# Kernel tuning notes

Hardware: AMD Instinct MI355X
Metric: run time of the kernel (lower is better)

The kernel has to match this reference:

```python
import jax, jax.numpy as jnp
import numpy as np

B, S, D, E = 8, 2048, 1024, 8
TOKENS = B * S
CAPACITY = TOKENS // E  # capacity_factor=1.0, top-1 gating (deepspeed default)


def _moe_layer(x_flat, Wg, We, be):
    """DeepSpeed-style top-1 MoE: gate -> capacity drop -> dispatch -> expert GEMM -> combine.
    x_flat: [T, D]; Wg: [D, E]; We: [E, D, D]; be: [E, D]."""
    gates = jax.nn.softmax(x_flat @ Wg, axis=-1)              # [T, E]
    idx = jnp.argmax(gates, axis=1)                            # [T] expert per token
    mask = jax.nn.one_hot(idx, E, dtype=jnp.int32)             # [T, E]
    loc = jnp.cumsum(mask, axis=0) - 1                         # position within expert
    loc_s = jnp.sum(loc * mask, axis=1)                        # [T]
    keep = loc_s < CAPACITY                                    # capacity drop
    gate_s = jnp.sum(gates * mask.astype(gates.dtype), axis=1) * keep.astype(gates.dtype)
    slot = jnp.clip(loc_s, 0, CAPACITY - 1)
    # dispatch: scatter kept tokens into [E, C, D] buffer (slots are unique for kept tokens)
    disp = jnp.zeros((E, CAPACITY, D), x_flat.dtype).at[idx, slot].add(
        x_flat * keep[:, None].astype(x_flat.dtype))
    # grouped expert GEMM
    eo = jnp.einsum('ecd,edf->ecf', disp, We) + be[:, None, :]  # [E, C, D]
    # combine: gather each token's expert output, scale by its gate value
    return eo[idx, slot] * gate_s[:, None]                      # [T, D]


def reference(x, y, W1, b1, Wg2, We2, be2, Wg3, We3, be3):
    h = jnp.einsum('bsd,df->bsf', x, W1) + b1                  # dense pre-layer
    hf = h.reshape(TOKENS, D)
    o = _moe_layer(hf, Wg2, We2, be2)
    o = _moe_layer(o, Wg3, We3, be3)
    h = h + o.reshape(B, S, D)                                 # residual add
    sent = h.mean(axis=1)                                      # [B, D]
    logp = jax.nn.log_softmax(sent, axis=-1)
    return -jnp.mean(logp[jnp.arange(B), y])                   # CrossEntropyLoss


def setup_inputs() -> dict:
    key = jax.random.key(0)
    ks = jax.random.split(key, 10)
    s = 0.02
    return {
        'x': jax.random.normal(ks[0], (B, S, D), jnp.float32),
        'y': jax.random.randint(ks[1], (B,), 0, D),
        'W1': jax.random.normal(ks[2], (D, D), jnp.float32) * s,
        'b1': jnp.zeros((D,), jnp.float32),
        'Wg2': jax.random.normal(ks[3], (D, E), jnp.float32) * s,
        'We2': jax.random.normal(ks[4], (E, D, D), jnp.float32) * s,
        'be2': jnp.zeros((E, D), jnp.float32),
        'Wg3': jax.random.normal(ks[5], (D, E), jnp.float32) * s,
        'We3': jax.random.normal(ks[6], (E, D, D), jnp.float32) * s,
        'be3': jnp.zeros((E, D), jnp.float32),
    }
```

## Files before the change

### kernel.cpp

```cpp
#include <hip/hip_runtime.h>
#include <hip/hip_bf16.h>
#include <math.h>


#define TOKS 16384
#define DIM 1024
#define NEXP 8
#define CAP 2048
#define BATCH 8
#define SEQ 2048

typedef __bf16 bf16_t;
typedef __bf16 bf16x8 __attribute__((ext_vector_type(8)));
typedef float fx4 __attribute__((ext_vector_type(4)));

__device__ __forceinline__ void gll16(const bf16_t* g, bf16_t* l) {
  __builtin_amdgcn_global_load_lds(
      (const __attribute__((address_space(1))) unsigned int*)g,
      (__attribute__((address_space(3))) unsigned int*)l, 16, 0, 0);
}

#define BARRIER() asm volatile("s_barrier" ::: "memory")
#define LGKM0()   asm volatile("s_waitcnt lgkmcnt(0)" ::: "memory")
#define VMC(N)    asm volatile("s_waitcnt vmcnt(" #N ")" ::: "memory")

#define PW_BLOCKS (17 * 64)
__global__ __launch_bounds__(256) void k_prep_w(
    const float* __restrict__ W1, const float* __restrict__ We2,
    const float* __restrict__ We3, bf16_t* __restrict__ Wt) {
  __shared__ bf16_t T[256][68];
  const int id = blockIdx.x;
  const int tid = threadIdx.x;
  const int m = id >> 6, rem = id & 63;
  const int k0 = (rem >> 4) * 256, n0 = (rem & 15) * 64;
  const float* src = (m == 0) ? W1
                     : (m <= 8) ? We2 + (size_t)(m - 1) * DIM * DIM
                                : We3 + (size_t)(m - 9) * DIM * DIM;
  bf16_t* dst = Wt + (size_t)m * DIM * DIM;
  const int r = tid >> 4, nq = tid & 15;
#pragma unroll
  for (int i = 0; i < 16; i++) {
    const int k = i * 16 + r;
    float4 v = *(const float4*)&src[(size_t)(k0 + k) * DIM + n0 + nq * 4];
    union { bf16_t h[4]; uint2 u; } t;
    t.h[0] = (bf16_t)v.x; t.h[1] = (bf16_t)v.y;
    t.h[2] = (bf16_t)v.z; t.h[3] = (bf16_t)v.w;
    *(uint2*)&T[k][(nq ^ ((k >> 3) & 15)) << 2] = t.u;
  }
  __syncthreads();
#pragma unroll
  for (int p = 0; p < 8; p++) {
    const int idx2 = p * 256 + tid;
    const int nl = idx2 >> 5, ks = (idx2 & 31) * 8;
    union { bf16_t h[8]; uint4 u; } o;
#pragma unroll
    for (int j = 0; j < 8; j++) {
      const int k = ks + j;
      o.h[j] = T[k][((((nl >> 2) ^ ((k >> 3) & 15)) << 2) | (nl & 3))];
    }
    *(uint4*)&dst[(size_t)(n0 + nl) * DIM + k0 + ks] = o.u;
  }
}

#define CVT_BLOCKS (TOKS * DIM / 8 / 256)
#define PREPX_GRID (2 + CVT_BLOCKS + 1)
__global__ __launch_bounds__(256) void k_prep_x(
    const float* __restrict__ Wg2, const float* __restrict__ Wg3,
    const float* __restrict__ x, bf16_t* __restrict__ WgP,
    bf16_t* __restrict__ xb, uint4* __restrict__ zreg, int znq) {
  const int id = blockIdx.x;
  const int tid = threadIdx.x;
  if (id < 2) {
    const int which = id;
    const float* src = which ? Wg3 : Wg2;
    bf16_t* dst = WgP + which * (128 * 8 * 8);
#pragma unroll
    for (int j = 0; j < 4; j++) {
      int d = tid * 4 + j;
      float4 a = *(const float4*)&src[d * 8];
      float4 b = *(const float4*)&src[d * 8 + 4];
      float v[8] = {a.x, a.y, a.z, a.w, b.x, b.y, b.z, b.w};
#pragma unroll
      for (int e = 0; e < 8; e++)
        dst[((d >> 3) * 8 + e) * 8 + (d & 7)] = (bf16_t)v[e];
    }
  } else if (id < 2 + CVT_BLOCKS) {
    const int cid = id - 2;
    size_t i = ((size_t)cid * 256 + tid) * 8;
    float4 a = *(const float4*)&x[i];
    float4 b = *(const float4*)&x[i + 4];
    union { bf16_t h[8]; uint4 u; } t;
    t.h[0] = (bf16_t)a.x; t.h[1] = (bf16_t)a.y; t.h[2] = (bf16_t)a.z; t.h[3] = (bf16_t)a.w;
    t.h[4] = (bf16_t)b.x; t.h[5] = (bf16_t)b.y; t.h[6] = (bf16_t)b.z; t.h[7] = (bf16_t)b.w;
    *(uint4*)&xb[i] = t.u;
  } else {
    const uint4 z = {0u, 0u, 0u, 0u};
    for (int i = tid; i < znq; i += 256) zreg[i] = z;
  }
}

template <int MODE>
__global__ __launch_bounds__(512) void k_gemm256(
    const bf16_t* __restrict__ A, const bf16_t* __restrict__ Bt0,
    const float* __restrict__ bias0, bf16_t* __restrict__ out,
    float* __restrict__ sent, const int* __restrict__ tok,
    const int* __restrict__ cnt, const float* __restrict__ gate,
    const bf16_t* __restrict__ zp) {
  __shared__ alignas(16) bf16_t As[2][256 * 64];
  __shared__ alignas(16) bf16_t Bs[2][256 * 64];
  const int tid = threadIdx.x;
  const int lane = tid & 63, wave = tid >> 6;
  const int quad = lane >> 4, l15 = lane & 15;
  const int wm = wave >> 2, wn = wave & 3;
  const int id = blockIdx.x;
  const int xcd = id & 7, rem = id >> 3;
  const int n0 = (rem & 3) * 256;

  int m0;
  int count = 0;
  const bf16_t* Bt;
  const float* bias;
  const int* tk = nullptr;
  if constexpr (MODE == 0) {
    m0 = (xcd * 8 + (rem >> 2)) * 256;
    Bt = Bt0;
    bias = bias0;
  } else {
    m0 = (rem >> 2) * 256;
    count = cnt[xcd];
    if (m0 >= count) return;
    Bt = Bt0 + (size_t)xcd * DIM * DIM;
    bias = bias0 + xcd * DIM;
    tk = tok + xcd * CAP;
  }

  const int kc = (tid & 7) ^ ((tid >> 3) & 7);
  const int rbase = tid >> 3;

  const bf16_t* gA[4];
  const bf16_t* gB[4];
#pragma unroll
  for (int h = 0; h < 2; h++)
#pragma unroll
    for (int i = 0; i < 2; i++) {
      const int r = h * 128 + i * 64 + rbase;
      if constexpr (MODE == 0) {
        gA[h * 2 + i] = A + (size_t)(m0 + r) * DIM + kc * 8;
      } else {
        const int ca = m0 + r;
        gA[h * 2 + i] = (ca < count) ? A + (size_t)tk[ca] * DIM + kc * 8 : zp;
      }
      gB[h * 2 + i] = Bt + (size_t)(n0 + r) * DIM + kc * 8;
    }

  auto stA = [&](int t, int half) {
#pragma unroll
    for (int i = 0; i < 2; i++)
      gll16(gA[half * 2 + i] + t * 64,
            &As[t & 1][(half * 128 + i * 64 + wave * 8) * 64]);
  };
  auto stB = [&](int t, int half) {
#pragma unroll
    for (int i = 0; i < 2; i++)
      gll16(gB[half * 2 + i] + t * 64,
            &Bs[t & 1][(half * 128 + i * 64 + wave * 8) * 64]);
  };
  auto rdA = [&](bf16x8 (&av)[4][2], int buf, int mh) {
#pragma unroll
    for (int mf = 0; mf < 4; mf++)
#pragma unroll
      for (int s = 0; s < 2; s++)
        av[mf][s] = *(const bf16x8*)&As[buf][(wm * 128 + (mh * 4 + mf) * 16 + l15) * 64 +
                                            (((s * 4 + quad) ^ (l15 & 7)) << 3)];
  };
  auto rdB = [&](bf16x8 (&bv)[2][2], int buf, int nh) {
#pragma unroll
    for (int nf = 0; nf < 2; nf++)
#pragma unroll
      for (int s = 0; s < 2; s++)
        bv[nf][s] = *(const bf16x8*)&Bs[buf][(wn * 64 + (nh * 2 + nf) * 16 + l15) * 64 +
                                            (((s * 4 + quad) ^ (l15 & 7)) << 3)];
  };

  fx4 acc[8][4];
#pragma unroll
  for (int i = 0; i < 8; i++)
#pragma unroll
    for (int j = 0; j < 4; j++) acc[i][j] = (fx4)0.0f;

  auto mma = [&](bf16x8 (&av)[4][2], bf16x8 (&bv)[2][2], int mh, int nh) {
    __builtin_amdgcn_s_setprio(1);
#pragma unroll
    for (int s = 0; s < 2; s++)
#pragma unroll
      for (int mf = 0; mf < 4; mf++)
#pragma unroll
        for (int nf = 0; nf < 2; nf++)
          acc[mh * 4 + mf][nh * 2 + nf] = __builtin_amdgcn_mfma_f32_16x16x32_bf16(
              av[mf][s], bv[nf][s], acc[mh * 4 + mf][nh * 2 + nf], 0, 0, 0);
    __builtin_amdgcn_s_setprio(0);
  };

  stA(0, 0); stA(0, 1); stB(0, 0); stB(0, 1);
  stB(1, 0); stB(1, 1); stA(1, 0);
  VMC(6);
  BARRIER();

  bf16x8 av0[4][2], av1[4][2], bv0[2][2], bv1[2][2];
#pragma unroll 2
  for (int t = 0; t < 14; t++) {
    const int buf = t & 1;
    rdA(av0, buf, 0); rdB(bv0, buf, 0); rdB(bv1, buf, 1);
    stA(t + 1, 1);
    BARRIER(); LGKM0();
    mma(av0, bv0, 0, 0);
    BARRIER();
    stB(t + 2, 0);
    BARRIER();
    mma(av0, bv1, 0, 1);
    BARRIER();
    rdA(av1, buf, 1);
    stB(t + 2, 1);
    BARRIER(); LGKM0();
    mma(av1, bv1, 1, 1);
    BARRIER();
    stA(t + 2, 0);
    mma(av1, bv0, 1, 0);
    VMC(6);
    BARRIER();
  }
  {
    rdA(av0, 0, 0); rdB(bv0, 0, 0); rdB(bv1, 0, 1);
    stA(15, 1);
    BARRIER(); LGKM0();
    mma(av0, bv0, 0, 0);
    BARRIER();
    mma(av0, bv1, 0, 1);
    BARRIER();
    rdA(av1, 0, 1);
    BARRIER(); LGKM0();
    mma(av1, bv1, 1, 1);
    BARRIER();
    mma(av1, bv0, 1, 0);
    VMC(0);
    BARRIER();
  }
  {
    rdA(av0, 1, 0); rdB(bv0, 1, 0); rdB(bv1, 1, 1); rdA(av1, 1, 1);
    LGKM0();
    mma(av0, bv0, 0, 0); mma(av0, bv1, 0, 1);
    mma(av1, bv1, 1, 1); mma(av1, bv0, 1, 0);
  }

  float bb[4];
#pragma unroll
  for (int nf = 0; nf < 4; nf++) bb[nf] = bias[n0 + wn * 64 + nf * 16 + l15];
  if constexpr (MODE == 0) {
    float sj[4] = {0.f, 0.f, 0.f, 0.f};
#pragma unroll
    for (int mf = 0; mf < 8; mf++)
#pragma unroll
      for (int r = 0; r < 4; r++) {
        const int rowL = wm * 128 + mf * 16 + quad * 4 + r;
#pragma unroll
        for (int nf = 0; nf < 4; nf++) {
          const float v = acc[mf][nf][r] + bb[nf];
          sj[nf] += v;
          out[(size_t)(m0 + rowL) * DIM + n0 + wn * 64 + nf * 16 + l15] = (bf16_t)v;
        }
      }
#pragma unroll
    for (int nf = 0; nf < 4; nf++) {
      sj[nf] += __shfl_xor(sj[nf], 16);
      sj[nf] += __shfl_xor(sj[nf], 32);
    }
    if (quad == 0)
#pragma unroll
      for (int nf = 0; nf < 4; nf++)
        atomicAdd(&sent[(m0 >> 11) * DIM + n0 + wn * 64 + nf * 16 + l15],
                  sj[nf] * (1.0f / SEQ));
  } else {
#pragma unroll
    for (int mf = 0; mf < 8; mf++)
#pragma unroll
      for (int r = 0; r < 4; r++) {
        const int c = m0 + wm * 128 + mf * 16 + quad * 4 + r;
        if (c < count) {
          const int tkn = tk[c];
          const float g = gate[tkn];
#pragma unroll
          for (int nf = 0; nf < 4; nf++)
            out[(size_t)tkn * DIM + n0 + wn * 64 + nf * 16 + l15] =
                (bf16_t)((acc[mf][nf][r] + bb[nf]) * g);
        }
      }
  }
}

__global__ __launch_bounds__(256) void k_gate_mm(
    const bf16_t* __restrict__ act, const bf16_t* __restrict__ WgPx,
    int* __restrict__ idx, float* __restrict__ gate) {
  __shared__ alignas(16) bf16_t As[64 * 64];
  __shared__ alignas(16) bf16_t WgS[128 * 64];
  __shared__ float L[64][8];
  const int tid = threadIdx.x;
  const int lane = tid & 63, wave = tid >> 6;
  const int quad = lane >> 4, l15 = lane & 15;
  const int m0 = blockIdx.x * 64;
  const int kc = (tid & 7) ^ ((tid >> 3) & 7);
  const int rbase = tid >> 3;

#pragma unroll
  for (int j = 0; j < 4; j++)
    gll16(WgPx + (j * 256 + wave * 64 + lane) * 8, &WgS[(j * 256 + wave * 64) * 8]);

  const bf16_t* gA[2]; bf16_t* lA[2];
#pragma unroll
  for (int i = 0; i < 2; i++) {
    gA[i] = act + (size_t)(m0 + rbase + 32 * i) * DIM + kc * 8;
    lA[i] = &As[wave * 512 + i * 2048];
  }
  fx4 acc = (fx4)0.0f;
  for (int k0 = 0; k0 < DIM; k0 += 64) {
#pragma unroll
    for (int i = 0; i < 2; i++) gll16(gA[i] + k0, lA[i]);
    __syncthreads();
#pragma unroll
    for (int s = 0; s < 2; s++) {
      const int pofs = ((s * 4 + quad) ^ (l15 & 7)) << 3;
      bf16x8 av = *(const bf16x8*)&As[(wave * 16 + l15) * 64 + pofs];
      bf16x8 bv = *(const bf16x8*)&WgS[((k0 >> 3) + s * 4 + quad) * 64 + (l15 & 7) * 8];
      acc = __builtin_amdgcn_mfma_f32_16x16x32_bf16(av, bv, acc, 0, 0, 0);
    }
    __syncthreads();
  }
  if (l15 < 8) {
#pragma unroll
    for (int r = 0; r < 4; r++) L[wave * 16 + quad * 4 + r][l15] = acc[r];
  }
  __syncthreads();
  if (tid < 64) {
    float lg[8];
#pragma unroll
    for (int e = 0; e < 8; e++) lg[e] = L[tid][e];
    float best = lg[0];
    int bi = 0;
#pragma unroll
    for (int e = 1; e < 8; e++)
      if (lg[e] > best) { best = lg[e]; bi = e; }
    float s = 0.f;
#pragma unroll
    for (int e = 0; e < 8; e++) s += expf(lg[e] - best);
    idx[m0 + tid] = bi;
    gate[m0 + tid] = 1.0f / s;
  }
}

#define DLMAX 2048
__global__ __launch_bounds__(1024) void k_route(
    const int* __restrict__ idx, int* __restrict__ tok, int* __restrict__ cnt,
    bf16_t* __restrict__ obuf) {
  const int e = blockIdx.x;
  const int tid = threadIdx.x, lane = tid & 63, wv = tid >> 6;
  __shared__ int wsum[16];
  __shared__ int dlist[DLMAX];
  const int4* p = (const int4*)(idx + tid * 16);
  int m[16];
  int c = 0;
#pragma unroll
  for (int j = 0; j < 4; j++) {
    int4 v = p[j];
    m[j * 4 + 0] = (v.x == e);
    m[j * 4 + 1] = (v.y == e);
    m[j * 4 + 2] = (v.z == e);
    m[j * 4 + 3] = (v.w == e);
    c += m[j * 4] + m[j * 4 + 1] + m[j * 4 + 2] + m[j * 4 + 3];
  }
  int sc = c;
#pragma unroll
  for (int off = 1; off < 64; off <<= 1) {
    int n = __shfl_up(sc, off);
    if (lane >= off) sc += n;
  }
  if (lane == 63) wsum[wv] = sc;
  __syncthreads();
  int wb = 0, tot = 0;
#pragma unroll
  for (int i = 0; i < 16; i++) {
    int s = wsum[i];
    tot += s;
    if (i < wv) wb += s;
  }
  int pos = wb + sc - c;
  const uint4 z = {0u, 0u, 0u, 0u};
#pragma unroll
  for (int j = 0; j < 16; j++) {
    if (m[j]) {
      int t = tid * 16 + j;
      if (pos < CAP) {
        tok[e * CAP + pos] = t;
      } else {
        int di = pos - CAP;
        if (di < DLMAX) dlist[di] = t;
        else
          for (int k = 0; k < 128; k++) *(uint4*)&obuf[(size_t)t * DIM + k * 8] = z;
      }
      pos++;
    }
  }
  if (tid == 0) cnt[e] = tot < CAP ? tot : CAP;
  __syncthreads();
  int ndl = tot - CAP;
  ndl = ndl < 0 ? 0 : (ndl > DLMAX ? DLMAX : ndl);
  for (int d = tid >> 7; d < ndl; d += 8) {
    int t = dlist[d];
    *(uint4*)&obuf[(size_t)t * DIM + (tid & 127) * 8] = z;
  }
}

__global__ __launch_bounds__(256) void k_reduce_loss(
    const bf16_t* __restrict__ o2, const float* __restrict__ sent,
    float* __restrict__ sentP, float* __restrict__ sentF,
    const int* __restrict__ y, int* __restrict__ done,
    float* __restrict__ out) {
  const int tid = threadIdx.x;
  const int job = blockIdx.x;
  const int b = job >> 6;
  __shared__ float lds[2][DIM];
  {
    const int d8 = (tid & 127) * 8;
    const int sg = tid >> 7;
    const int s0 = (job & 63) * 32 + sg * 16;
    float acc[8] = {0.f, 0.f, 0.f, 0.f, 0.f, 0.f, 0.f, 0.f};
    const size_t base = ((size_t)b * SEQ + s0) * DIM + d8;
#pragma unroll 1
    for (int i0 = 0; i0 < 16; i0 += 8) {
      uint4 u[8];
#pragma unroll
      for (int i = 0; i < 8; i++)
        u[i] = *(const uint4*)&o2[base + (size_t)(i0 + i) * DIM];
#pragma unroll
      for (int i = 0; i < 8; i++) {
        union { bf16_t v[8]; uint4 q; } oo;
        oo.q = u[i];
#pragma unroll
        for (int j = 0; j < 8; j++) acc[j] += (float)oo.v[j];
      }
    }
#pragma unroll
    for (int j = 0; j < 8; j++) lds[sg][d8 + j] = acc[j];
  }
  __syncthreads();
  {
    const int c4 = tid * 4;
    float4 s;
    s.x = lds[0][c4] + lds[1][c4];
    s.y = lds[0][c4 + 1] + lds[1][c4 + 1];
    s.z = lds[0][c4 + 2] + lds[1][c4 + 2];
    s.w = lds[0][c4 + 3] + lds[1][c4 + 3];
    *(float4*)&sentP[(size_t)job * DIM + c4] = s;
  }
  __shared__ int isLastB;
  __syncthreads();
  if (tid == 0) {
    __threadfence();
    isLastB = (atomicAdd(&done[b], 1) == 63);
  }
  __syncthreads();
  if (!isLastB) return;
  __threadfence();
  {
    const int c4 = tid * 4;
    float4 t4 = {0.f, 0.f, 0.f, 0.f};
    const float* pb = sentP + (size_t)(b * 64) * DIM + c4;
#pragma unroll 1
    for (int r0 = 0; r0 < 64; r0 += 8) {
      float4 u[8];
#pragma unroll
      for (int r = 0; r < 8; r++) u[r] = *(const float4*)&pb[(size_t)(r0 + r) * DIM];
#pragma unroll
      for (int r = 0; r < 8; r++) {
        t4.x += u[r].x; t4.y += u[r].y; t4.z += u[r].z; t4.w += u[r].w;
      }
    }
    float4 s4 = *(const float4*)&sent[b * DIM + c4];
    float4 f;
    f.x = s4.x + t4.x * (1.0f / SEQ);
    f.y = s4.y + t4.y * (1.0f / SEQ);
    f.z = s4.z + t4.z * (1.0f / SEQ);
    f.w = s4.w + t4.w * (1.0f / SEQ);
    *(float4*)&sentF[b * DIM + c4] = f;
  }
  __shared__ int isLastF;
  __syncthreads();
  if (tid == 0) {
    __threadfence();
    isLastF = (atomicAdd(&done[8], 1) == 7);
  }
  __syncthreads();
  if (!isLastF) return;
  __threadfence();
  __shared__ float red[256];
  float total = 0.f;
  for (int bb = 0; bb < BATCH; bb++) {
    const int c4 = tid * 4;
    float4 f = *(const float4*)&sentF[bb * DIM + c4];
    float m = fmaxf(fmaxf(f.x, f.y), fmaxf(f.z, f.w));
    red[tid] = m;
    __syncthreads();
    for (int s = 128; s; s >>= 1) {
      if (tid < s) red[tid] = fmaxf(red[tid], red[tid + s]);
      __syncthreads();
    }
    m = red[0];
    __syncthreads();
    float sum = expf(f.x - m) + expf(f.y - m) + expf(f.z - m) + expf(f.w - m);
    red[tid] = sum;
    __syncthreads();
    for (int s = 128; s; s >>= 1) {
      if (tid < s) red[tid] += red[tid + s];
      __syncthreads();
    }
    if (tid == 0) total += m + logf(red[0]) - sentF[bb * DIM + y[bb]];
    __syncthreads();
  }
  if (tid == 0) out[0] = total * (1.0f / BATCH);
}

extern "C" void kernel_launch(void* const* d_in, const int* in_sizes, int n_in,
                              void* d_out, int out_size, void* d_ws, size_t ws_size,
                              hipStream_t stream) {
  (void)in_sizes; (void)n_in; (void)out_size; (void)ws_size;
  const float* x   = (const float*)d_in[0];
  const int*   y   = (const int*)d_in[1];
  const float* W1  = (const float*)d_in[2];
  const float* b1  = (const float*)d_in[3];
  const float* Wg2 = (const float*)d_in[4];
  const float* We2 = (const float*)d_in[5];
  const float* be2 = (const float*)d_in[6];
  const float* Wg3 = (const float*)d_in[7];
  const float* We3 = (const float*)d_in[8];
  const float* be3 = (const float*)d_in[9];

  char* p = (char*)d_ws;
  size_t off = 0;
  auto carve = [&](size_t bytes) -> char* {
    char* r = p + off;
    off += (bytes + 255) & ~(size_t)255;
    return r;
  };
  bf16_t* Wt   = (bf16_t*)carve((size_t)17 * DIM * DIM * 2);
  bf16_t* WgP  = (bf16_t*)carve(2 * 128 * 8 * 8 * 2);
  bf16_t* h    = (bf16_t*)carve((size_t)TOKS * DIM * 2);
  bf16_t* o1   = (bf16_t*)carve((size_t)TOKS * DIM * 2);
  bf16_t* o2   = (bf16_t*)carve((size_t)TOKS * DIM * 2);
  int*    idx  = (int*)carve(TOKS * 4);
  float*  gate = (float*)carve(TOKS * 4);
  int*    tok  = (int*)carve(NEXP * CAP * 4);
  int*    cnt  = (int*)carve(NEXP * 4);
  size_t zoff0 = off;
  float*  sent = (float*)carve(BATCH * DIM * 4);
  bf16_t* zp   = (bf16_t*)carve(4096);
  int*    done = (int*)carve(256);
  size_t zbytes = off - zoff0;
  float*  sentP = (float*)carve((size_t)512 * DIM * 4);
  float*  sentF = (float*)carve((size_t)BATCH * DIM * 4);
  bf16_t* xb   = o2;

  k_prep_w<<<PW_BLOCKS, 256, 0, stream>>>(W1, We2, We3, Wt);
  k_prep_x<<<PREPX_GRID, 256, 0, stream>>>(
      Wg2, Wg3, x, WgP, xb, (uint4*)sent, (int)(zbytes / 16));

  k_gemm256<0><<<256, 512, 0, stream>>>(
      xb, Wt, b1, h, sent, nullptr, nullptr, nullptr, zp);

  k_gate_mm<<<TOKS / 64, 256, 0, stream>>>(h, WgP, idx, gate);
  k_route<<<NEXP, 1024, 0, stream>>>(idx, tok, cnt, o1);
  k_gemm256<1><<<256, 512, 0, stream>>>(
      h, Wt + (size_t)1 * DIM * DIM, be2, o1, nullptr, tok, cnt, gate, zp);

  k_gate_mm<<<TOKS / 64, 256, 0, stream>>>(o1, WgP + 128 * 8 * 8, idx, gate);
  k_route<<<NEXP, 1024, 0, stream>>>(idx, tok, cnt, o2);
  k_gemm256<1><<<256, 512, 0, stream>>>(
      o1, Wt + (size_t)9 * DIM * DIM, be3, o2, nullptr, tok, cnt, gate, zp);

  k_reduce_loss<<<512, 256, 0, stream>>>(o2, sent, sentP, sentF, y, done,
                                         (float*)d_out);
}
```

Measured before the change: 376.4 us.

## Shrink GEMM tile to 128x256 with triple-buffered LDS pipeline and double grid

The GEMM block tile drops from 256x256 to 128x256, the grid doubles to 512 blocks, and the split half-stage double-buffer schedule becomes a simpler three-stage ring where each iteration issues one full stage load and then computes one tile. This targets low occupancy and wave quantization from having only 256 large blocks, and removes the many intra-iteration barriers. The cost is lower operand reuse per block and more B-matrix traffic. The reduce-loss kernel is also split into twice as many jobs with half the rows each.

```diff
diff --git a/kernel.cpp b/kernel.cpp
--- a/kernel.cpp
+++ b/kernel.cpp
@@ -21,7 +21,6 @@
 }
 
 #define BARRIER() asm volatile("s_barrier" ::: "memory")
-#define LGKM0()   asm volatile("s_waitcnt lgkmcnt(0)" ::: "memory")
 #define VMC(N)    asm volatile("s_waitcnt vmcnt(" #N ")" ::: "memory")
 
 #define PW_BLOCKS (17 * 64)
@@ -106,8 +105,8 @@
     float* __restrict__ sent, const int* __restrict__ tok,
     const int* __restrict__ cnt, const float* __restrict__ gate,
     const bf16_t* __restrict__ zp) {
-  __shared__ alignas(16) bf16_t As[2][256 * 64];
-  __shared__ alignas(16) bf16_t Bs[2][256 * 64];
+  __shared__ alignas(16) bf16_t As[3][128 * 64];
+  __shared__ alignas(16) bf16_t Bs[3][256 * 64];
   const int tid = threadIdx.x;
   const int lane = tid & 63, wave = tid >> 6;
   const int quad = lane >> 4, l15 = lane & 15;
@@ -122,11 +121,11 @@
   const float* bias;
   const int* tk = nullptr;
   if constexpr (MODE == 0) {
-    m0 = (xcd * 8 + (rem >> 2)) * 256;
+    m0 = (xcd * 16 + (rem >> 2)) * 128;
     Bt = Bt0;
     bias = bias0;
   } else {
-    m0 = (rem >> 2) * 256;
+    m0 = (rem >> 2) * 128;
     count = cnt[xcd];
     if (m0 >= count) return;
     Bt = Bt0 + (size_t)xcd * DIM * DIM;
@@ -137,120 +136,85 @@
   const int kc = (tid & 7) ^ ((tid >> 3) & 7);
   const int rbase = tid >> 3;
 
-  const bf16_t* gA[4];
+  const bf16_t* gA[2];
   const bf16_t* gB[4];
 #pragma unroll
-  for (int h = 0; h < 2; h++)
-#pragma unroll
-    for (int i = 0; i < 2; i++) {
-      const int r = h * 128 + i * 64 + rbase;
-      if constexpr (MODE == 0) {
-        gA[h * 2 + i] = A + (size_t)(m0 + r) * DIM + kc * 8;
-      } else {
-        const int ca = m0 + r;
-        gA[h * 2 + i] = (ca < count) ? A + (size_t)tk[ca] * DIM + kc * 8 : zp;
-      }
-      gB[h * 2 + i] = Bt + (size_t)(n0 + r) * DIM + kc * 8;
-    }
-
-  auto stA = [&](int t, int half) {
+  for (int i = 0; i < 2; i++) {
+    const int r = i * 64 + rbase;
+    if constexpr (MODE == 0) {
+      gA[i] = A + (size_t)(m0 + r) * DIM + kc * 8;
+    } else {
+      const int ca = m0 + r;
+      gA[i] = (ca < count) ? A + (size_t)tk[ca] * DIM + kc * 8 : zp;
+    }
+  }
+#pragma unroll
+  for (int i = 0; i < 4; i++)
+    gB[i] = Bt + (size_t)(n0 + i * 64 + rbase) * DIM + kc * 8;
+
+  auto stage = [&](int t, int bufi) {
 #pragma unroll
     for (int i = 0; i < 2; i++)
-      gll16(gA[half * 2 + i] + t * 64,
-            &As[t & 1][(half * 128 + i * 64 + wave * 8) * 64]);
+      gll16(gA[i] + t * 64, &As[bufi][(i * 64 + wave * 8) * 64]);
+#pragma unroll
+    for (int i = 0; i < 4; i++)
+      gll16(gB[i] + t * 64, &Bs[bufi][(i * 64 + wave * 8) * 64]);
   };
-  auto stB = [&](int t, int half) {
-#pragma unroll
-    for (int i = 0; i < 2; i++)
-      gll16(gB[half * 2 + i] + t * 64,
-            &Bs[t & 1][(half * 128 + i * 64 + wave * 8) * 64]);
+
+  fx4 acc[4][4];
+#pragma unroll
+  for (int i = 0; i < 4; i++)
+#pragma unroll
+    for (int j = 0; j < 4; j++) acc[i][j] = (fx4)0.0f;
+
+  auto tilecomp = [&](int bufi) {
+    bf16x8 av[4][2], bv[4][2];
+#pragma unroll
+    for (int mf = 0; mf < 4; mf++)
+#pragma unroll
+      for (int s = 0; s < 2; s++)
+        av[mf][s] = *(const bf16x8*)&As[bufi][(wm * 64 + mf * 16 + l15) * 64 +
+                                             (((s * 4 + quad) ^ (l15 & 7)) << 3)];
+#pragma unroll
+    for (int nf = 0; nf < 4; nf++)
+#pragma unroll
+      for (int s = 0; s < 2; s++)
+        bv[nf][s] = *(const bf16x8*)&Bs[bufi][(wn * 64 + nf * 16 + l15) * 64 +
+                                             (((s * 4 + quad) ^ (l15 & 7)) << 3)];
+    __builtin_amdgcn_s_setprio(1);
+#pragma unroll
+    for (int s = 0; s < 2; s++)
+#pragma unroll
+      for (int mf = 0; mf < 4; mf++)
+#pragma unroll
+        for (int nf = 0; nf < 4; nf++)
+          acc[mf][nf] = __builtin_amdgcn_mfma_f32_16x16x32_bf16(
+              av[mf][s], bv[nf][s], acc[mf][nf], 0, 0, 0);
+    __builtin_amdgcn_s_setprio(0);
+    __builtin_amdgcn_sched_barrier(0);
   };
-  auto rdA = [&](bf16x8 (&av)[4][2], int buf, int mh) {
-#pragma unroll
-    for (int mf = 0; mf < 4; mf++)
-#pragma unroll
-      for (int s = 0; s < 2; s++)
-        av[mf][s] = *(const bf16x8*)&As[buf][(wm * 128 + (mh * 4 + mf) * 16 + l15) * 64 +
-                                            (((s * 4 + quad) ^ (l15 & 7)) << 3)];
-  };
-  auto rdB = [&](bf16x8 (&bv)[2][2], int buf, int nh) {
-#pragma unroll
-    for (int nf = 0; nf < 2; nf++)
-#pragma unroll
-      for (int s = 0; s < 2; s++)
-        bv[nf][s] = *(const bf16x8*)&Bs[buf][(wn * 64 + (nh * 2 + nf) * 16 + l15) * 64 +
-                                            (((s * 4 + quad) ^ (l15 & 7)) << 3)];
-  };
-
-  fx4 acc[8][4];
-#pragma unroll
-  for (int i = 0; i < 8; i++)
-#pragma unroll
-    for (int j = 0; j < 4; j++) acc[i][j] = (fx4)0.0f;
-
-  auto mma = [&](bf16x8 (&av)[4][2], bf16x8 (&bv)[2][2], int mh, int nh) {
-    __builtin_amdgcn_s_setprio(1);
-#pragma unroll
-    for (int s = 0; s < 2; s++)
-#pragma unroll
-      for (int mf = 0; mf < 4; mf++)
-#pragma unroll
-        for (int nf = 0; nf < 2; nf++)
-          acc[mh * 4 + mf][nh * 2 + nf] = __builtin_amdgcn_mfma_f32_16x16x32_bf16(
-              av[mf][s], bv[nf][s], acc[mh * 4 + mf][nh * 2 + nf], 0, 0, 0);
-    __builtin_amdgcn_s_setprio(0);
-  };
-
-  stA(0, 0); stA(0, 1); stB(0, 0); stB(0, 1);
-  stB(1, 0); stB(1, 1); stA(1, 0);
+
+  stage(0, 0);
+  stage(1, 1);
   VMC(6);
   BARRIER();
 
-  bf16x8 av0[4][2], av1[4][2], bv0[2][2], bv1[2][2];
-#pragma unroll 2
+  int cur = 0;
+#pragma unroll 1
   for (int t = 0; t < 14; t++) {
-    const int buf = t & 1;
-    rdA(av0, buf, 0); rdB(bv0, buf, 0); rdB(bv1, buf, 1);
-    stA(t + 1, 1);
-    BARRIER(); LGKM0();
-    mma(av0, bv0, 0, 0);
-    BARRIER();
-    stB(t + 2, 0);
-    BARRIER();
-    mma(av0, bv1, 0, 1);
-    BARRIER();
-    rdA(av1, buf, 1);
-    stB(t + 2, 1);
-    BARRIER(); LGKM0();
-    mma(av1, bv1, 1, 1);
-    BARRIER();
-    stA(t + 2, 0);
-    mma(av1, bv0, 1, 0);
+    int b2 = cur + 2;
+    if (b2 >= 3) b2 -= 3;
+    stage(t + 2, b2);
+    tilecomp(cur);
     VMC(6);
     BARRIER();
-  }
-  {
-    rdA(av0, 0, 0); rdB(bv0, 0, 0); rdB(bv1, 0, 1);
-    stA(15, 1);
-    BARRIER(); LGKM0();
-    mma(av0, bv0, 0, 0);
-    BARRIER();
-    mma(av0, bv1, 0, 1);
-    BARRIER();
-    rdA(av1, 0, 1);
-    BARRIER(); LGKM0();
-    mma(av1, bv1, 1, 1);
-    BARRIER();
-    mma(av1, bv0, 1, 0);
-    VMC(0);
-    BARRIER();
-  }
-  {
-    rdA(av0, 1, 0); rdB(bv0, 1, 0); rdB(bv1, 1, 1); rdA(av1, 1, 1);
-    LGKM0();
-    mma(av0, bv0, 0, 0); mma(av0, bv1, 0, 1);
-    mma(av1, bv1, 1, 1); mma(av1, bv0, 1, 0);
-  }
+    cur = cur + 1;
+    if (cur == 3) cur = 0;
+  }
+  tilecomp(2);
+  VMC(0);
+  BARRIER();
+  tilecomp(0);
 
   float bb[4];
 #pragma unroll
@@ -258,10 +222,10 @@
   if constexpr (MODE == 0) {
     float sj[4] = {0.f, 0.f, 0.f, 0.f};
 #pragma unroll
-    for (int mf = 0; mf < 8; mf++)
+    for (int mf = 0; mf < 4; mf++)
 #pragma unroll
       for (int r = 0; r < 4; r++) {
-        const int rowL = wm * 128 + mf * 16 + quad * 4 + r;
+        const int rowL = wm * 64 + mf * 16 + quad * 4 + r;
 #pragma unroll
         for (int nf = 0; nf < 4; nf++) {
           const float v = acc[mf][nf][r] + bb[nf];
@@ -281,10 +245,10 @@
                   sj[nf] * (1.0f / SEQ));
   } else {
 #pragma unroll
-    for (int mf = 0; mf < 8; mf++)
+    for (int mf = 0; mf < 4; mf++)
 #pragma unroll
       for (int r = 0; r < 4; r++) {
-        const int c = m0 + wm * 128 + mf * 16 + quad * 4 + r;
+        const int c = m0 + wm * 64 + mf * 16 + quad * 4 + r;
         if (c < count) {
           const int tkn = tk[c];
           const float g = gate[tkn];
@@ -425,27 +389,24 @@
     float* __restrict__ out) {
   const int tid = threadIdx.x;
   const int job = blockIdx.x;
-  const int b = job >> 6;
+  const int b = job >> 7;
   __shared__ float lds[2][DIM];
   {
     const int d8 = (tid & 127) * 8;
     const int sg = tid >> 7;
-    const int s0 = (job & 63) * 32 + sg * 16;
+    const int s0 = (job & 127) * 16 + sg * 8;
     float acc[8] = {0.f, 0.f, 0.f, 0.f, 0.f, 0.f, 0.f, 0.f};
     const size_t base = ((size_t)b * SEQ + s0) * DIM + d8;
-#pragma unroll 1
-    for (int i0 = 0; i0 < 16; i0 += 8) {
-      uint4 u[8];
-#pragma unroll
-      for (int i = 0; i < 8; i++)
-        u[i] = *(const uint4*)&o2[base + (size_t)(i0 + i) * DIM];
-#pragma unroll
-      for (int i = 0; i < 8; i++) {
-        union { bf16_t v[8]; uint4 q; } oo;
-        oo.q = u[i];
-#pragma unroll
-        for (int j = 0; j < 8; j++) acc[j] += (float)oo.v[j];
-      }
+    uint4 u[8];
+#pragma unroll
+    for (int i = 0; i < 8; i++)
+      u[i] = *(const uint4*)&o2[base + (size_t)i * DIM];
+#pragma unroll
+    for (int i = 0; i < 8; i++) {
+      union { bf16_t v[8]; uint4 q; } oo;
+      oo.q = u[i];
+#pragma unroll
+      for (int j = 0; j < 8; j++) acc[j] += (float)oo.v[j];
     }
 #pragma unroll
     for (int j = 0; j < 8; j++) lds[sg][d8 + j] = acc[j];
@@ -464,7 +425,7 @@
   __syncthreads();
   if (tid == 0) {
     __threadfence();
-    isLastB = (atomicAdd(&done[b], 1) == 63);
+    isLastB = (atomicAdd(&done[b], 1) == 127);
   }
   __syncthreads();
   if (!isLastB) return;
@@ -472,9 +433,9 @@
   {
     const int c4 = tid * 4;
     float4 t4 = {0.f, 0.f, 0.f, 0.f};
-    const float* pb = sentP + (size_t)(b * 64) * DIM + c4;
+    const float* pb = sentP + (size_t)(b * 128) * DIM + c4;
 #pragma unroll 1
-    for (int r0 = 0; r0 < 64; r0 += 8) {
+    for (int r0 = 0; r0 < 128; r0 += 8) {
       float4 u[8];
 #pragma unroll
       for (int r = 0; r < 8; r++) u[r] = *(const float4*)&pb[(size_t)(r0 + r) * DIM];
@@ -563,7 +524,7 @@
   bf16_t* zp   = (bf16_t*)carve(4096);
   int*    done = (int*)carve(256);
   size_t zbytes = off - zoff0;
-  float*  sentP = (float*)carve((size_t)512 * DIM * 4);
+  float*  sentP = (float*)carve((size_t)1024 * DIM * 4);
   float*  sentF = (float*)carve((size_t)BATCH * DIM * 4);
   bf16_t* xb   = o2;
 
@@ -571,19 +532,19 @@
   k_prep_x<<<PREPX_GRID, 256, 0, stream>>>(
       Wg2, Wg3, x, WgP, xb, (uint4*)sent, (int)(zbytes / 16));
 
-  k_gemm256<0><<<256, 512, 0, stream>>>(
+  k_gemm256<0><<<512, 512, 0, stream>>>(
       xb, Wt, b1, h, sent, nullptr, nullptr, nullptr, zp);
 
   k_gate_mm<<<TOKS / 64, 256, 0, stream>>>(h, WgP, idx, gate);
   k_route<<<NEXP, 1024, 0, stream>>>(idx, tok, cnt, o1);
-  k_gemm256<1><<<256, 512, 0, stream>>>(
+  k_gemm256<1><<<512, 512, 0, stream>>>(
       h, Wt + (size_t)1 * DIM * DIM, be2, o1, nullptr, tok, cnt, gate, zp);
 
   k_gate_mm<<<TOKS / 64, 256, 0, stream>>>(o1, WgP + 128 * 8 * 8, idx, gate);
   k_route<<<NEXP, 1024, 0, stream>>>(idx, tok, cnt, o2);
-  k_gemm256<1><<<256, 512, 0, stream>>>(
+  k_gemm256<1><<<512, 512, 0, stream>>>(
       o1, Wt + (size_t)9 * DIM * DIM, be3, o2, nullptr, tok, cnt, gate, zp);
 
-  k_reduce_loss<<<512, 256, 0, stream>>>(o2, sent, sentP, sentF, y, done,
-                                         (float*)d_out);
-}
+  k_reduce_loss<<<1024, 256, 0, stream>>>(o2, sent, sentP, sentF, y, done,
+                                          (float*)d_out);
+}
```

After: 443.6 us. 1.18x slower.

## Fuse second MoE combine with per-batch sequence-mean reduction into expert GEMM epilogue

Applied to the files above, without the earlier changes.

The final expert GEMM no longer writes its output tokens to a bf16 buffer. Its epilogue now accumulates gated outputs per batch into LDS with shared atomics and writes one per-block partial slab. A small k_sum kernel adds the slabs to the dense residual mean, and a single-block kernel computes the loss. This removes the full 32MB write and re-read of o2 and the multi-stage done-counter reduction, at the cost of LDS atomic contention in the epilogue and extra small launches. The route kernel still zeroes dropped tokens in o2, though nothing reads them now, and o2 still holds the converted input, so this stays correct.

```diff
diff --git a/kernel.cpp b/kernel.cpp
--- a/kernel.cpp
+++ b/kernel.cpp
@@ -105,9 +105,10 @@
     const float* __restrict__ bias0, bf16_t* __restrict__ out,
     float* __restrict__ sent, const int* __restrict__ tok,
     const int* __restrict__ cnt, const float* __restrict__ gate,
-    const bf16_t* __restrict__ zp) {
+    const bf16_t* __restrict__ zp, float* __restrict__ slabs) {
   __shared__ alignas(16) bf16_t As[2][256 * 64];
   __shared__ alignas(16) bf16_t Bs[2][256 * 64];
+  __shared__ float sacc[MODE == 2 ? 8 * 256 : 1];
   const int tid = threadIdx.x;
   const int lane = tid & 63, wave = tid >> 6;
   const int quad = lane >> 4, l15 = lane & 15;
@@ -115,6 +116,10 @@
   const int id = blockIdx.x;
   const int xcd = id & 7, rem = id >> 3;
   const int n0 = (rem & 3) * 256;
+
+  if constexpr (MODE == 2) {
+    for (int i = tid; i < 2048; i += 512) sacc[i] = 0.f;
+  }
 
   int m0;
   int count = 0;
@@ -128,7 +133,13 @@
   } else {
     m0 = (rem >> 2) * 256;
     count = cnt[xcd];
-    if (m0 >= count) return;
+    if (m0 >= count) {
+      if constexpr (MODE == 2) {
+        float* slab = slabs + (size_t)id * 2048;
+        for (int i = tid; i < 2048; i += 512) slab[i] = 0.f;
+      }
+      return;
+    }
     Bt = Bt0 + (size_t)xcd * DIM * DIM;
     bias = bias0 + xcd * DIM;
     tk = tok + xcd * CAP;
@@ -279,7 +290,7 @@
       for (int nf = 0; nf < 4; nf++)
         atomicAdd(&sent[(m0 >> 11) * DIM + n0 + wn * 64 + nf * 16 + l15],
                   sj[nf] * (1.0f / SEQ));
-  } else {
+  } else if constexpr (MODE == 1) {
 #pragma unroll
     for (int mf = 0; mf < 8; mf++)
 #pragma unroll
@@ -294,6 +305,25 @@
                 (bf16_t)((acc[mf][nf][r] + bb[nf]) * g);
         }
       }
+  } else {
+#pragma unroll
+    for (int mf = 0; mf < 8; mf++)
+#pragma unroll
+      for (int r = 0; r < 4; r++) {
+        const int c = m0 + wm * 128 + mf * 16 + quad * 4 + r;
+        if (c < count) {
+          const int tkn = tk[c];
+          const float g = gate[tkn];
+          const int b = tkn >> 11;
+#pragma unroll
+          for (int nf = 0; nf < 4; nf++)
+            atomicAdd(&sacc[b * 256 + wn * 64 + nf * 16 + l15],
+                      (acc[mf][nf][r] + bb[nf]) * g);
+        }
+      }
+    __syncthreads();
+    float* slab = slabs + (size_t)id * 2048;
+    for (int i = tid; i < 2048; i += 512) slab[i] = sacc[i];
   }
 }
 
@@ -418,93 +448,32 @@
   }
 }
 
-__global__ __launch_bounds__(256) void k_reduce_loss(
-    const bf16_t* __restrict__ o2, const float* __restrict__ sent,
-    float* __restrict__ sentP, float* __restrict__ sentF,
-    const int* __restrict__ y, int* __restrict__ done,
+__global__ __launch_bounds__(256) void k_sum(
+    const float* __restrict__ slabs, const float* __restrict__ sent,
+    float* __restrict__ sentF) {
+  const int b = blockIdx.x >> 2, sub = blockIdx.x & 3;
+  const int tid = threadIdx.x;
+  float a = 0.f;
+#pragma unroll 1
+  for (int rg = 0; rg < 8; rg++) {
+    const int rem = rg * 4 + sub;
+#pragma unroll
+    for (int xcd = 0; xcd < 8; xcd++)
+      a += slabs[(size_t)(rem * 8 + xcd) * 2048 + b * 256 + tid];
+  }
+  const int col = sub * 256 + tid;
+  sentF[b * DIM + col] = sent[b * DIM + col] + a * (1.0f / SEQ);
+}
+
+__global__ __launch_bounds__(256) void k_loss(
+    const float* __restrict__ sentF, const int* __restrict__ y,
     float* __restrict__ out) {
   const int tid = threadIdx.x;
-  const int job = blockIdx.x;
-  const int b = job >> 6;
-  __shared__ float lds[2][DIM];
-  {
-    const int d8 = (tid & 127) * 8;
-    const int sg = tid >> 7;
-    const int s0 = (job & 63) * 32 + sg * 16;
-    float acc[8] = {0.f, 0.f, 0.f, 0.f, 0.f, 0.f, 0.f, 0.f};
-    const size_t base = ((size_t)b * SEQ + s0) * DIM + d8;
-#pragma unroll 1
-    for (int i0 = 0; i0 < 16; i0 += 8) {
-      uint4 u[8];
-#pragma unroll
-      for (int i = 0; i < 8; i++)
-        u[i] = *(const uint4*)&o2[base + (size_t)(i0 + i) * DIM];
-#pragma unroll
-      for (int i = 0; i < 8; i++) {
-        union { bf16_t v[8]; uint4 q; } oo;
-        oo.q = u[i];
-#pragma unroll
-        for (int j = 0; j < 8; j++) acc[j] += (float)oo.v[j];
-      }
-    }
-#pragma unroll
-    for (int j = 0; j < 8; j++) lds[sg][d8 + j] = acc[j];
-  }
-  __syncthreads();
-  {
-    const int c4 = tid * 4;
-    float4 s;
-    s.x = lds[0][c4] + lds[1][c4];
-    s.y = lds[0][c4 + 1] + lds[1][c4 + 1];
-    s.z = lds[0][c4 + 2] + lds[1][c4 + 2];
-    s.w = lds[0][c4 + 3] + lds[1][c4 + 3];
-    *(float4*)&sentP[(size_t)job * DIM + c4] = s;
-  }
-  __shared__ int isLastB;
-  __syncthreads();
-  if (tid == 0) {
-    __threadfence();
-    isLastB = (atomicAdd(&done[b], 1) == 63);
-  }
-  __syncthreads();
-  if (!isLastB) return;
-  __threadfence();
-  {
-    const int c4 = tid * 4;
-    float4 t4 = {0.f, 0.f, 0.f, 0.f};
-    const float* pb = sentP + (size_t)(b * 64) * DIM + c4;
-#pragma unroll 1
-    for (int r0 = 0; r0 < 64; r0 += 8) {
-      float4 u[8];
-#pragma unroll
-      for (int r = 0; r < 8; r++) u[r] = *(const float4*)&pb[(size_t)(r0 + r) * DIM];
-#pragma unroll
-      for (int r = 0; r < 8; r++) {
-        t4.x += u[r].x; t4.y += u[r].y; t4.z += u[r].z; t4.w += u[r].w;
-      }
-    }
-    float4 s4 = *(const float4*)&sent[b * DIM + c4];
-    float4 f;
-    f.x = s4.x + t4.x * (1.0f / SEQ);
-    f.y = s4.y + t4.y * (1.0f / SEQ);
-    f.z = s4.z + t4.z * (1.0f / SEQ);
-    f.w = s4.w + t4.w * (1.0f / SEQ);
-    *(float4*)&sentF[b * DIM + c4] = f;
-  }
-  __shared__ int isLastF;
-  __syncthreads();
-  if (tid == 0) {
-    __threadfence();
-    isLastF = (atomicAdd(&done[8], 1) == 7);
-  }
-  __syncthreads();
-  if (!isLastF) return;
-  __threadfence();
   __shared__ float red[256];
   float total = 0.f;
-  for (int bb = 0; bb < BATCH; bb++) {
+  for (int b = 0; b < BATCH; b++) {
     const int c4 = tid * 4;
-    float4 f = *(const float4*)&sentF[bb * DIM + c4];
+    float4 f = *(const float4*)&sentF[b * DIM + c4];
     float m = fmaxf(fmaxf(f.x, f.y), fmaxf(f.z, f.w));
     red[tid] = m;
     __syncthreads();
@@ -521,7 +490,7 @@
       if (tid < s) red[tid] += red[tid + s];
       __syncthreads();
     }
-    if (tid == 0) total += m + logf(red[0]) - sentF[bb * DIM + y[bb]];
+    if (tid == 0) total += m + logf(red[0]) - sentF[b * DIM + y[b]];
     __syncthreads();
   }
   if (tid == 0) out[0] = total * (1.0f / BATCH);
@@ -561,9 +530,8 @@
   size_t zoff0 = off;
   float*  sent = (float*)carve(BATCH * DIM * 4);
   bf16_t* zp   = (bf16_t*)carve(4096);
-  int*    done = (int*)carve(256);
   size_t zbytes = off - zoff0;
-  float*  sentP = (float*)carve((size_t)512 * DIM * 4);
+  float*  slabs = (float*)carve((size_t)256 * 2048 * 4);
   float*  sentF = (float*)carve((size_t)BATCH * DIM * 4);
   bf16_t* xb   = o2;
 
@@ -572,18 +540,18 @@
       Wg2, Wg3, x, WgP, xb, (uint4*)sent, (int)(zbytes / 16));
 
   k_gemm256<0><<<256, 512, 0, stream>>>(
-      xb, Wt, b1, h, sent, nullptr, nullptr, nullptr, zp);
+      xb, Wt, b1, h, sent, nullptr, nullptr, nullptr, zp, nullptr);
 
   k_gate_mm<<<TOKS / 64, 256, 0, stream>>>(h, WgP, idx, gate);
   k_route<<<NEXP, 1024, 0, stream>>>(idx, tok, cnt, o1);
   k_gemm256<1><<<256, 512, 0, stream>>>(
-      h, Wt + (size_t)1 * DIM * DIM, be2, o1, nullptr, tok, cnt, gate, zp);
+      h, Wt + (size_t)1 * DIM * DIM, be2, o1, nullptr, tok, cnt, gate, zp, nullptr);
 
   k_gate_mm<<<TOKS / 64, 256, 0, stream>>>(o1, WgP + 128 * 8 * 8, idx, gate);
   k_route<<<NEXP, 1024, 0, stream>>>(idx, tok, cnt, o2);
-  k_gemm256<1><<<256, 512, 0, stream>>>(
-      o1, Wt + (size_t)9 * DIM * DIM, be3, o2, nullptr, tok, cnt, gate, zp);
-
-  k_reduce_loss<<<512, 256, 0, stream>>>(o2, sent, sentP, sentF, y, done,
-                                         (float*)d_out);
-}
+  k_gemm256<2><<<256, 512, 0, stream>>>(
+      o1, Wt + (size_t)9 * DIM * DIM, be3, nullptr, nullptr, tok, cnt, gate, zp, slabs);
+
+  k_sum<<<32, 256, 0, stream>>>(slabs, sent, sentF);
+  k_loss<<<1, 256, 0, stream>>>(sentF, y, (float*)d_out);
+}
```

After: 414.4 us. 1.1x slower.
